# Optimization experiments

Measured on AMD Instinct MI355X. Metric: run time of the kernel, lower is better.

Reference implementation:

```python
import jax, jax.numpy as jnp
import numpy as np

N_DFT = 512
N_FILTER = N_DFT // 2 + 1  # 257
N_HOP = N_DFT // 2         # 256
AMIN = 1e-10
DYNAMIC_RANGE = 80.0


def _dft_kernels(n_dft):
    """Windowed real-DFT kernels, shape (n_dft, n_filter) each."""
    n_filter = n_dft // 2 + 1
    n = np.arange(n_dft)
    # periodic Hann (scipy.signal.hann(n_dft, sym=False))
    win = 0.5 - 0.5 * np.cos(2.0 * np.pi * n / n_dft)
    ang = 2.0 * np.pi * np.outer(n, np.arange(n_filter)) / n_dft  # (n_dft, n_filter)
    k_real = (np.cos(ang) * win[:, None]).astype(np.float32)
    k_imag = (np.sin(ang) * win[:, None]).astype(np.float32)
    return jnp.asarray(k_real), jnp.asarray(k_imag)


def setup_inputs() -> dict:
    key = jax.random.key(0)
    x = jax.random.normal(key, (32, 2, 262144), dtype=jnp.float32)  # (batch, ch, samples)
    k_real, k_imag = _dft_kernels(N_DFT)
    return {"x": x, "k_real": k_real, "k_imag": k_imag}


def reference(x, k_real, k_imag):
    n_dft = k_real.shape[0]
    n_hop = n_dft // 2
    B, C, L = x.shape
    # TF/Keras 'same' padding with stride n_hop
    n_frame = -(-L // n_hop)
    rem = L % n_hop
    pad_total = max(n_dft - n_hop, 0) if rem == 0 else max(n_dft - rem, 0)
    pad_l = pad_total // 2
    xp = jnp.pad(x, ((0, 0), (0, 0), (pad_l, pad_total - pad_l)))
    # frame the signal: (B, C, n_frame, n_dft)
    idx = jnp.arange(n_frame)[:, None] * n_hop + jnp.arange(n_dft)[None, :]
    frames = xp[:, :, idx]
    # DFT via dense GEMM with cos/sin kernels
    re = jnp.einsum('bctd,df->bctf', frames, k_real)
    im = jnp.einsum('bctd,df->bctf', frames, k_imag)
    power = re * re + im * im  # (B, C, n_frame, n_filter)
    # channels_last output: (B, n_freq, n_time, n_ch)
    out = jnp.transpose(power, (0, 3, 2, 1))
    # power_spectrogram == 2.0 -> no pow adjustment; decibel conversion:
    log10 = jnp.float32(np.log(10.0))
    log_spec = 10.0 * jnp.log(jnp.maximum(out, AMIN)) / log10
    log_spec = log_spec - jnp.max(log_spec)
    return jnp.maximum(log_spec, -DYNAMIC_RANGE)
```

## Files before the change

### kernel.cpp

```cpp
#include <hip/hip_runtime.h>
#include <math.h>

#define L_IN     262144
#define N_FRAME  1024
#define AMIN     1e-10f
#define DRANGE   80.0f
#define UNITS_CH 1056
#define WS_HI_OFF   4096
#define WS_HALF     524288
#define N4_OUT   ((32 * 257 * 1024 * 2) / 4)

typedef short bf16x8 __attribute__((ext_vector_type(8)));
typedef short bf16x4 __attribute__((ext_vector_type(4)));
typedef float f32x16 __attribute__((ext_vector_type(16)));

__device__ __forceinline__ short f2bf(float f) {
    unsigned u = __float_as_uint(f);
    u = (u + 0x7FFFu + ((u >> 16) & 1u)) >> 16;
    return (short)u;
}
__device__ __forceinline__ float bf2f(short h) {
    return __uint_as_float(((unsigned)(unsigned short)h) << 16);
}
__device__ __forceinline__ int swz(int u) { return u ^ ((u >> 5) & 7); }

__global__ __launch_bounds__(256) void wconv_kernel(
    const float* __restrict__ kr, const float* __restrict__ ki,
    short* __restrict__ whi, short* __restrict__ wlo, unsigned* __restrict__ wsmax)
{
    if (blockIdx.x == 0 && threadIdx.x == 0) wsmax[0] = 0u;
    const int tid  = threadIdx.x;
    const int pair = blockIdx.x * 4 + (tid >> 6);
    const int lane = tid & 63;
    const int fi = pair >> 5, kk = pair & 31;
    const int g = fi >> 1, nf = fi & 1;
    const int n  = lane & 31;
    const int k0 = kk * 16 + (lane >> 5) * 8;
    const int f  = g * 32 + n;
    bf16x8 h8, l8;
    #pragma unroll
    for (int j = 0; j < 8; ++j) {
        const int k = k0 + j;
        float w;
        if (nf == 1 && g == 0 && n == 0) w = kr[k * 257 + 256];
        else                             w = (nf ? ki : kr)[k * 257 + f];
        short hh = f2bf(w);
        h8[j] = hh;
        l8[j] = f2bf(w - bf2f(hh));
    }
    const int off = ((fi * 32 + kk) * 64 + lane) * 8;
    *(bf16x8*)(whi + off) = h8;
    *(bf16x8*)(wlo + off) = l8;
}

__global__ __launch_bounds__(512, 4) void spec_kernel(
    const float* __restrict__ x,
    const short* __restrict__ whi, const short* __restrict__ wlo,
    float* __restrict__ out, unsigned* __restrict__ wsmax)
{
    __shared__ __align__(16) char smem[2 * 2 * UNITS_CH * 8 * sizeof(short)];
    __shared__ float wmax[8];
    short* Ah = (short*)smem;
    short* Al = (short*)(smem + 2 * UNITS_CH * 8 * sizeof(short));
    float* S  = (float*)smem;

    const int blk = blockIdx.x;
    const int tt  = blk & 31;
    const int b   = blk >> 5;
    const int tid = threadIdx.x;
    const int lane = tid & 63;
    const int g    = tid >> 6;
    const int col  = lane & 31;
    const int half = lane >> 5;

    const int s_origin = tt * 8192 - 128;
    for (int cc = g; cc < 66; cc += 8) {
        const int ch   = (cc >= 33) ? 1 : 0;
        const int c    = cc - ch * 33;
        const int base = s_origin + c * 256;
        const float* xp = x + ((size_t)b * 2 + ch) * L_IN;
        const int i4 = base + lane * 4;
        float v[4];
        if (base >= 0 && base + 256 <= L_IN) {
            float4 p = *(const float4*)(xp + i4);
            v[0] = p.x; v[1] = p.y; v[2] = p.z; v[3] = p.w;
        } else {
            #pragma unroll
            for (int j = 0; j < 4; ++j) {
                const int idx = i4 + j;
                v[j] = (idx >= 0 && idx < L_IN) ? xp[idx] : 0.0f;
            }
        }
        bf16x4 h4, l4;
        #pragma unroll
        for (int j = 0; j < 4; ++j) {
            short hh = f2bf(v[j]);
            h4[j] = hh;
            l4[j] = f2bf(v[j] - bf2f(hh));
        }
        const int u = c * 32 + (lane >> 1);
        const int e = (ch * UNITS_CH + swz(u)) * 8 + (lane & 1) * 4;
        *(bf16x4*)&Ah[e] = h4;
        *(bf16x4*)&Al[e] = l4;
    }
    __syncthreads();

    f32x16 acc[2][2];
    #pragma unroll
    for (int mf = 0; mf < 2; ++mf)
        #pragma unroll
        for (int nf = 0; nf < 2; ++nf)
            #pragma unroll
            for (int r = 0; r < 16; ++r) acc[mf][nf][r] = 0.0f;

    const int laneoff = lane * 8;
    const short* whiW = whi + (g * 2) * 32 * 64 * 8 + laneoff;
    const short* wloW = wlo + (g * 2) * 32 * 64 * 8 + laneoff;

    for (int kk = 0; kk < 32; ++kk) {
        const int u0 = col * 32 + kk * 2 + half;
        const int e0 = swz(u0) * 8;
        const int e1 = (UNITS_CH + swz(u0)) * 8;
        const int wo = kk * 64 * 8;
        bf16x8 bh0 = *(const bf16x8*)(whiW + wo);
        bf16x8 bh1 = *(const bf16x8*)(whiW + 32 * 64 * 8 + wo);
        bf16x8 ah0 = *(const bf16x8*)&Ah[e0];
        bf16x8 ah1 = *(const bf16x8*)&Ah[e1];
        acc[0][0] = __builtin_amdgcn_mfma_f32_32x32x16_bf16(ah0, bh0, acc[0][0], 0, 0, 0);
        acc[0][1] = __builtin_amdgcn_mfma_f32_32x32x16_bf16(ah0, bh1, acc[0][1], 0, 0, 0);
        acc[1][0] = __builtin_amdgcn_mfma_f32_32x32x16_bf16(ah1, bh0, acc[1][0], 0, 0, 0);
        acc[1][1] = __builtin_amdgcn_mfma_f32_32x32x16_bf16(ah1, bh1, acc[1][1], 0, 0, 0);
        bf16x8 bl0 = *(const bf16x8*)(wloW + wo);
        bf16x8 bl1 = *(const bf16x8*)(wloW + 32 * 64 * 8 + wo);
        acc[0][0] = __builtin_amdgcn_mfma_f32_32x32x16_bf16(ah0, bl0, acc[0][0], 0, 0, 0);
        acc[0][1] = __builtin_amdgcn_mfma_f32_32x32x16_bf16(ah0, bl1, acc[0][1], 0, 0, 0);
        acc[1][0] = __builtin_amdgcn_mfma_f32_32x32x16_bf16(ah1, bl0, acc[1][0], 0, 0, 0);
        acc[1][1] = __builtin_amdgcn_mfma_f32_32x32x16_bf16(ah1, bl1, acc[1][1], 0, 0, 0);
        bf16x8 al0 = *(const bf16x8*)&Al[e0];
        bf16x8 al1 = *(const bf16x8*)&Al[e1];
        acc[0][0] = __builtin_amdgcn_mfma_f32_32x32x16_bf16(al0, bh0, acc[0][0], 0, 0, 0);
        acc[0][1] = __builtin_amdgcn_mfma_f32_32x32x16_bf16(al0, bh1, acc[0][1], 0, 0, 0);
        acc[1][0] = __builtin_amdgcn_mfma_f32_32x32x16_bf16(al1, bh0, acc[1][0], 0, 0, 0);
        acc[1][1] = __builtin_amdgcn_mfma_f32_32x32x16_bf16(al1, bh1, acc[1][1], 0, 0, 0);
    }

    __syncthreads();
    const bool nyq = (g == 0) && (col == 0);
    float pmax = 0.0f;
    #pragma unroll
    for (int mf = 0; mf < 2; ++mf) {
        #pragma unroll
        for (int r = 0; r < 16; ++r) {
            const int m   = (r & 3) + 8 * (r >> 2) + 4 * half;
            const int row = m * 2 + mf;
            const float re = acc[mf][0][r];
            const float im = acc[mf][1][r];
            const float imq = nyq ? 0.0f : im;
            float p = fmaxf(re * re + imq * imq, AMIN);
            pmax = fmaxf(pmax, p);
            S[row * 257 + g * 32 + col] = p;
            if (nyq) {
                float pn = fmaxf(im * im, AMIN);
                pmax = fmaxf(pmax, pn);
                S[row * 257 + 256] = pn;
            }
        }
    }
    #pragma unroll
    for (int off = 32; off > 0; off >>= 1)
        pmax = fmaxf(pmax, __shfl_down(pmax, off, 64));
    if (lane == 0) wmax[g] = pmax;
    __syncthreads();
    if (tid == 0) {
        float m2 = wmax[0];
        #pragma unroll
        for (int w = 1; w < 8; ++w) m2 = fmaxf(m2, wmax[w]);
        atomicMax(wsmax, __float_as_uint(m2));
    }
    float* obase = out + (size_t)b * 526336 + (size_t)tt * 64;
    for (int q = tid; q < 257 * 16; q += 512) {
        const int f = q >> 4, part = q & 15;
        float4 vv;
        vv.x = S[(part * 4 + 0) * 257 + f];
        vv.y = S[(part * 4 + 1) * 257 + f];
        vv.z = S[(part * 4 + 2) * 257 + f];
        vv.w = S[(part * 4 + 3) * 257 + f];
        *(float4*)(obase + (size_t)f * 2048 + part * 4) = vv;
    }
}

__global__ __launch_bounds__(256) void finalize_kernel(
    float* __restrict__ out, const unsigned* __restrict__ ws_max, int n4)
{
    const int i = blockIdx.x * 256 + threadIdx.x;
    if (i >= n4) return;
    const float mlog = 10.0f * log10f(__uint_as_float(*ws_max));
    float4 p = ((const float4*)out)[i];
    float4 v;
    v.x = fmaxf(10.0f * log10f(p.x) - mlog, -DRANGE);
    v.y = fmaxf(10.0f * log10f(p.y) - mlog, -DRANGE);
    v.z = fmaxf(10.0f * log10f(p.z) - mlog, -DRANGE);
    v.w = fmaxf(10.0f * log10f(p.w) - mlog, -DRANGE);
    ((float4*)out)[i] = v;
}

extern "C" void kernel_launch(void* const* d_in, const int* in_sizes, int n_in,
                              void* d_out, int out_size, void* d_ws, size_t ws_size,
                              hipStream_t stream) {
    const float* x  = (const float*)d_in[0];
    const float* kr = (const float*)d_in[1];
    const float* ki = (const float*)d_in[2];
    float* out      = (float*)d_out;

    unsigned* wsmax = (unsigned*)d_ws;
    short* whi      = (short*)((char*)d_ws + WS_HI_OFF);
    short* wlo      = (short*)((char*)d_ws + WS_HI_OFF + WS_HALF);

    wconv_kernel<<<128, 256, 0, stream>>>(kr, ki, whi, wlo, wsmax);

    const int nblocks = 32 * 32;
    spec_kernel<<<nblocks, 512, 0, stream>>>(x, whi, wlo, out, wsmax);

    const int n4 = N4_OUT;
    finalize_kernel<<<(n4 + 255) / 256, 256, 0, stream>>>(out, wsmax, n4);
}
```

Before: 214.6 us.

## Stream DFT weight tiles into LDS via async global_load_lds pipeline

Weight fragments are no longer read straight from global memory inside the MFMA loop. Each wave now issues direct global-to-LDS loads (global_load_lds) ahead of use, with a 3-stage ring for the hi weights and a 2-stage ring for the lo weights, and waits with a manual vmcnt. This is meant to hide global load latency behind the MFMA work. LDS use grows to about 146 KB and the occupancy hint in launch_bounds is dropped, so fewer blocks fit per CU. The loop also prefetches wrapped indices on the last iterations, which wastes some loads.

```diff
diff --git a/kernel.cpp b/kernel.cpp
--- a/kernel.cpp
+++ b/kernel.cpp
@@ -10,9 +10,20 @@
 #define WS_HALF     524288
 #define N4_OUT   ((32 * 257 * 1024 * 2) / 4)
 
+#define A_BYTES   67584
+#define WH_OFF    67584
+#define WL_OFF    116736
+#define SMEM_BYTES 149504
+
 typedef short bf16x8 __attribute__((ext_vector_type(8)));
 typedef short bf16x4 __attribute__((ext_vector_type(4)));
 typedef float f32x16 __attribute__((ext_vector_type(16)));
+
+typedef __attribute__((address_space(1))) const void av1_t;
+typedef __attribute__((address_space(3))) void av3_t;
+__device__ __forceinline__ void gload_lds16(const void* g, void* l) {
+    __builtin_amdgcn_global_load_lds((av1_t*)g, (av3_t*)l, 16, 0, 0);
+}
 
 __device__ __forceinline__ short f2bf(float f) {
     unsigned u = __float_as_uint(f);
@@ -53,15 +64,15 @@
     *(bf16x8*)(wlo + off) = l8;
 }
 
-__global__ __launch_bounds__(512, 4) void spec_kernel(
+__global__ __launch_bounds__(512) void spec_kernel(
     const float* __restrict__ x,
     const short* __restrict__ whi, const short* __restrict__ wlo,
     float* __restrict__ out, unsigned* __restrict__ wsmax)
 {
-    __shared__ __align__(16) char smem[2 * 2 * UNITS_CH * 8 * sizeof(short)];
+    __shared__ __align__(16) char smem[SMEM_BYTES];
     __shared__ float wmax[8];
     short* Ah = (short*)smem;
-    short* Al = (short*)(smem + 2 * UNITS_CH * 8 * sizeof(short));
+    short* Al = (short*)(smem + A_BYTES / 2);
     float* S  = (float*)smem;
 
     const int blk = blockIdx.x;
@@ -72,6 +83,16 @@
     const int g    = tid >> 6;
     const int col  = lane & 31;
     const int half = lane >> 5;
+
+    const short* wgH = whi + (g * 2) * 32 * 64 * 8 + lane * 8;
+    const short* wgL = wlo + (g * 2) * 32 * 64 * 8 + lane * 8;
+
+    gload_lds16(wgL,                 smem + WL_OFF + ((g * 2 + 0) * 2 + 0) * 1024);
+    gload_lds16(wgL + 16384,         smem + WL_OFF + ((g * 2 + 0) * 2 + 1) * 1024);
+    gload_lds16(wgH,                 smem + WH_OFF + ((g * 3 + 0) * 2 + 0) * 1024);
+    gload_lds16(wgH + 16384,         smem + WH_OFF + ((g * 3 + 0) * 2 + 1) * 1024);
+    gload_lds16(wgH + 512,           smem + WH_OFF + ((g * 3 + 1) * 2 + 0) * 1024);
+    gload_lds16(wgH + 16384 + 512,   smem + WH_OFF + ((g * 3 + 1) * 2 + 1) * 1024);
 
     const int s_origin = tt * 8192 - 128;
     for (int cc = g; cc < 66; cc += 8) {
@@ -113,35 +134,47 @@
             #pragma unroll
             for (int r = 0; r < 16; ++r) acc[mf][nf][r] = 0.0f;
 
-    const int laneoff = lane * 8;
-    const short* whiW = whi + (g * 2) * 32 * 64 * 8 + laneoff;
-    const short* wloW = wlo + (g * 2) * 32 * 64 * 8 + laneoff;
-
-    for (int kk = 0; kk < 32; ++kk) {
-        const int u0 = col * 32 + kk * 2 + half;
+    int d3 = 0;
+    for (int s = 0; s < 32; ++s) {
+        const int kkL = (s + 1) & 31;
+        const int kkH = (s + 2) & 31;
+        const int dL = (s + 1) & 1;
+        const int dH = (d3 == 0) ? 2 : d3 - 1;
+        gload_lds16(wgL + kkL * 512,         smem + WL_OFF + ((g * 2 + dL) * 2 + 0) * 1024);
+        gload_lds16(wgL + 16384 + kkL * 512, smem + WL_OFF + ((g * 2 + dL) * 2 + 1) * 1024);
+        gload_lds16(wgH + kkH * 512,         smem + WH_OFF + ((g * 3 + dH) * 2 + 0) * 1024);
+        gload_lds16(wgH + 16384 + kkH * 512, smem + WH_OFF + ((g * 3 + dH) * 2 + 1) * 1024);
+        asm volatile("s_waitcnt vmcnt(6)" ::: "memory");
+
+        const int hbase = WH_OFF + (g * 3 + d3) * 2048 + lane * 16;
+        const int lbase = WL_OFF + (g * 2 + (s & 1)) * 2048 + lane * 16;
+        bf16x8 bh0 = *(const bf16x8*)(smem + hbase);
+        bf16x8 bh1 = *(const bf16x8*)(smem + hbase + 1024);
+        bf16x8 bl0 = *(const bf16x8*)(smem + lbase);
+        bf16x8 bl1 = *(const bf16x8*)(smem + lbase + 1024);
+
+        const int u0 = col * 32 + s * 2 + half;
         const int e0 = swz(u0) * 8;
         const int e1 = (UNITS_CH + swz(u0)) * 8;
-        const int wo = kk * 64 * 8;
-        bf16x8 bh0 = *(const bf16x8*)(whiW + wo);
-        bf16x8 bh1 = *(const bf16x8*)(whiW + 32 * 64 * 8 + wo);
         bf16x8 ah0 = *(const bf16x8*)&Ah[e0];
         bf16x8 ah1 = *(const bf16x8*)&Ah[e1];
+        bf16x8 al0 = *(const bf16x8*)&Al[e0];
+        bf16x8 al1 = *(const bf16x8*)&Al[e1];
+
         acc[0][0] = __builtin_amdgcn_mfma_f32_32x32x16_bf16(ah0, bh0, acc[0][0], 0, 0, 0);
         acc[0][1] = __builtin_amdgcn_mfma_f32_32x32x16_bf16(ah0, bh1, acc[0][1], 0, 0, 0);
         acc[1][0] = __builtin_amdgcn_mfma_f32_32x32x16_bf16(ah1, bh0, acc[1][0], 0, 0, 0);
         acc[1][1] = __builtin_amdgcn_mfma_f32_32x32x16_bf16(ah1, bh1, acc[1][1], 0, 0, 0);
-        bf16x8 bl0 = *(const bf16x8*)(wloW + wo);
-        bf16x8 bl1 = *(const bf16x8*)(wloW + 32 * 64 * 8 + wo);
         acc[0][0] = __builtin_amdgcn_mfma_f32_32x32x16_bf16(ah0, bl0, acc[0][0], 0, 0, 0);
         acc[0][1] = __builtin_amdgcn_mfma_f32_32x32x16_bf16(ah0, bl1, acc[0][1], 0, 0, 0);
         acc[1][0] = __builtin_amdgcn_mfma_f32_32x32x16_bf16(ah1, bl0, acc[1][0], 0, 0, 0);
         acc[1][1] = __builtin_amdgcn_mfma_f32_32x32x16_bf16(ah1, bl1, acc[1][1], 0, 0, 0);
-        bf16x8 al0 = *(const bf16x8*)&Al[e0];
-        bf16x8 al1 = *(const bf16x8*)&Al[e1];
         acc[0][0] = __builtin_amdgcn_mfma_f32_32x32x16_bf16(al0, bh0, acc[0][0], 0, 0, 0);
         acc[0][1] = __builtin_amdgcn_mfma_f32_32x32x16_bf16(al0, bh1, acc[0][1], 0, 0, 0);
         acc[1][0] = __builtin_amdgcn_mfma_f32_32x32x16_bf16(al1, bh0, acc[1][0], 0, 0, 0);
         acc[1][1] = __builtin_amdgcn_mfma_f32_32x32x16_bf16(al1, bh1, acc[1][1], 0, 0, 0);
+
+        d3 = (d3 == 2) ? 0 : d3 + 1;
     }
 
     __syncthreads();
```

Result: slower. 242.3 us (+12.9%).

## Double-buffer weight and signal K-slices in LDS via async global-to-LDS loads

Applied to the files above, without the earlier changes.

The main loop now streams K-slices instead of staging the whole signal tile up front and reading weights straight from global memory in the MFMA loop. Weights are staged into an LDS double-buffer with global_load_lds, and each next signal slice is loaded and split into bf16 hi/lo during the current step's MFMAs. This targets global-load latency on the weight operands and the serial prologue. The cost is a barrier every K step, a smaller-footprint but different LDS layout without swizzling (possible bank conflicts), and dropping the occupancy hint in launch_bounds.

```diff
diff --git a/kernel.cpp b/kernel.cpp
--- a/kernel.cpp
+++ b/kernel.cpp
@@ -5,14 +5,22 @@
 #define N_FRAME  1024
 #define AMIN     1e-10f
 #define DRANGE   80.0f
-#define UNITS_CH 1056
 #define WS_HI_OFF   4096
 #define WS_HALF     524288
 #define N4_OUT   ((32 * 257 * 1024 * 2) / 4)
 
+#define ARING_OFF 0
+#define WRING_OFF 8192
+#define SMEM_BYTES 73728
+
 typedef short bf16x8 __attribute__((ext_vector_type(8)));
-typedef short bf16x4 __attribute__((ext_vector_type(4)));
 typedef float f32x16 __attribute__((ext_vector_type(16)));
+
+typedef __attribute__((address_space(1))) const void av1_t;
+typedef __attribute__((address_space(3))) void av3_t;
+__device__ __forceinline__ void gload_lds16(const void* g, void* l) {
+    __builtin_amdgcn_global_load_lds((av1_t*)g, (av3_t*)l, 16, 0, 0);
+}
 
 __device__ __forceinline__ short f2bf(float f) {
     unsigned u = __float_as_uint(f);
@@ -22,7 +30,6 @@
 __device__ __forceinline__ float bf2f(short h) {
     return __uint_as_float(((unsigned)(unsigned short)h) << 16);
 }
-__device__ __forceinline__ int swz(int u) { return u ^ ((u >> 5) & 7); }
 
 __global__ __launch_bounds__(256) void wconv_kernel(
     const float* __restrict__ kr, const float* __restrict__ ki,
@@ -53,16 +60,14 @@
     *(bf16x8*)(wlo + off) = l8;
 }
 
-__global__ __launch_bounds__(512, 4) void spec_kernel(
+__global__ __launch_bounds__(512) void spec_kernel(
     const float* __restrict__ x,
     const short* __restrict__ whi, const short* __restrict__ wlo,
     float* __restrict__ out, unsigned* __restrict__ wsmax)
 {
-    __shared__ __align__(16) char smem[2 * 2 * UNITS_CH * 8 * sizeof(short)];
+    __shared__ __align__(16) char smem[SMEM_BYTES];
     __shared__ float wmax[8];
-    short* Ah = (short*)smem;
-    short* Al = (short*)(smem + 2 * UNITS_CH * 8 * sizeof(short));
-    float* S  = (float*)smem;
+    float* S = (float*)smem;
 
     const int blk = blockIdx.x;
     const int tt  = blk & 31;
@@ -73,37 +78,43 @@
     const int col  = lane & 31;
     const int half = lane >> 5;
 
+    const short* wgH = whi + (g * 2) * 32 * 64 * 8 + lane * 8;
+    const short* wgL = wlo + (g * 2) * 32 * 64 * 8 + lane * 8;
+
     const int s_origin = tt * 8192 - 128;
-    for (int cc = g; cc < 66; cc += 8) {
-        const int ch   = (cc >= 33) ? 1 : 0;
-        const int c    = cc - ch * 33;
-        const int base = s_origin + c * 256;
-        const float* xp = x + ((size_t)b * 2 + ch) * L_IN;
-        const int i4 = base + lane * 4;
-        float v[4];
-        if (base >= 0 && base + 256 <= L_IN) {
-            float4 p = *(const float4*)(xp + i4);
-            v[0] = p.x; v[1] = p.y; v[2] = p.z; v[3] = p.w;
-        } else {
-            #pragma unroll
-            for (int j = 0; j < 4; ++j) {
-                const int idx = i4 + j;
-                v[j] = (idx >= 0 && idx < L_IN) ? xp[idx] : 0.0f;
-            }
-        }
-        bf16x4 h4, l4;
-        #pragma unroll
-        for (int j = 0; j < 4; ++j) {
-            short hh = f2bf(v[j]);
-            h4[j] = hh;
-            l4[j] = f2bf(v[j] - bf2f(hh));
-        }
-        const int u = c * 32 + (lane >> 1);
-        const int e = (ch * UNITS_CH + swz(u)) * 8 + (lane & 1) * 4;
-        *(bf16x4*)&Ah[e] = h4;
-        *(bf16x4*)&Al[e] = l4;
-    }
-    __syncthreads();
+    const int q    = tid >> 2;
+    const int j2   = (tid & 3) * 2;
+    const int mfst = q >> 6;
+    const int cc   = q & 63;
+    const int ubase = (cc >> 1) * 32 + (cc & 1);
+    const float* xst = x + ((size_t)b * 2 + mfst) * L_IN;
+    const int ibase = s_origin + ubase * 8 + j2;
+    const int a_waddr = q * 16 + (tid & 3) * 4;
+    const int ard0 = (col * 2 + half) * 16;
+    const int ard1 = (64 + col * 2 + half) * 16;
+
+    {
+        char* wb = smem + WRING_OFF + g * 4096;
+        gload_lds16(wgH,         wb);
+        gload_lds16(wgH + 16384, wb + 1024);
+        gload_lds16(wgL,         wb + 2048);
+        gload_lds16(wgL + 16384, wb + 3072);
+        const int i0 = ibase;
+        const bool o0 = (i0 >= 0) && (i0 < L_IN);
+        const bool o1 = (i0 + 1 >= 0) && (i0 + 1 < L_IN);
+        const int c0 = i0 < 0 ? 0 : (i0 >= L_IN ? L_IN - 1 : i0);
+        const int c1 = (i0 + 1) < 0 ? 0 : ((i0 + 1) >= L_IN ? L_IN - 1 : (i0 + 1));
+        float v0 = xst[c0]; if (!o0) v0 = 0.0f;
+        float v1 = xst[c1]; if (!o1) v1 = 0.0f;
+        short h0 = f2bf(v0), h1 = f2bf(v1);
+        short l0 = f2bf(v0 - bf2f(h0)), l1 = f2bf(v1 - bf2f(h1));
+        *(unsigned*)(smem + ARING_OFF + a_waddr) =
+            (unsigned)(unsigned short)h0 | ((unsigned)(unsigned short)h1 << 16);
+        *(unsigned*)(smem + ARING_OFF + 2048 + a_waddr) =
+            (unsigned)(unsigned short)l0 | ((unsigned)(unsigned short)l1 << 16);
+        asm volatile("s_waitcnt lgkmcnt(0)" ::: "memory");
+        __builtin_amdgcn_s_barrier();
+    }
 
     f32x16 acc[2][2];
     #pragma unroll
@@ -113,35 +124,62 @@
             #pragma unroll
             for (int r = 0; r < 16; ++r) acc[mf][nf][r] = 0.0f;
 
-    const int laneoff = lane * 8;
-    const short* whiW = whi + (g * 2) * 32 * 64 * 8 + laneoff;
-    const short* wloW = wlo + (g * 2) * 32 * 64 * 8 + laneoff;
-
-    for (int kk = 0; kk < 32; ++kk) {
-        const int u0 = col * 32 + kk * 2 + half;
-        const int e0 = swz(u0) * 8;
-        const int e1 = (UNITS_CH + swz(u0)) * 8;
-        const int wo = kk * 64 * 8;
-        bf16x8 bh0 = *(const bf16x8*)(whiW + wo);
-        bf16x8 bh1 = *(const bf16x8*)(whiW + 32 * 64 * 8 + wo);
-        bf16x8 ah0 = *(const bf16x8*)&Ah[e0];
-        bf16x8 ah1 = *(const bf16x8*)&Ah[e1];
+    int cur = 0;
+    for (int s = 0; s < 32; ++s) {
+        const int kkn = (s + 1) & 31;
+        const int nxt = cur ^ 1;
+        const int i0 = ibase + kkn * 16;
+        const bool o0 = (i0 >= 0) && (i0 < L_IN);
+        const bool o1 = (i0 + 1 >= 0) && (i0 + 1 < L_IN);
+        const int c0 = i0 < 0 ? 0 : (i0 >= L_IN ? L_IN - 1 : i0);
+        const int c1 = (i0 + 1) < 0 ? 0 : ((i0 + 1) >= L_IN ? L_IN - 1 : (i0 + 1));
+        const float v0 = xst[c0];
+        const float v1 = xst[c1];
+        {
+            char* wb = smem + WRING_OFF + (nxt * 8 + g) * 4096;
+            const short* wh = wgH + kkn * 512;
+            const short* wl = wgL + kkn * 512;
+            gload_lds16(wh,          wb);
+            gload_lds16(wh + 16384,  wb + 1024);
+            gload_lds16(wl,          wb + 2048);
+            gload_lds16(wl + 16384,  wb + 3072);
+        }
+        asm volatile("s_waitcnt vmcnt(6)" ::: "memory");
+        const char* wr = smem + WRING_OFF + (cur * 8 + g) * 4096 + lane * 16;
+        bf16x8 bh0 = *(const bf16x8*)(wr);
+        bf16x8 bh1 = *(const bf16x8*)(wr + 1024);
+        bf16x8 bl0 = *(const bf16x8*)(wr + 2048);
+        bf16x8 bl1 = *(const bf16x8*)(wr + 3072);
+        const char* ar = smem + ARING_OFF + cur * 4096;
+        bf16x8 ah0 = *(const bf16x8*)(ar + ard0);
+        bf16x8 ah1 = *(const bf16x8*)(ar + ard1);
+        bf16x8 al0 = *(const bf16x8*)(ar + 2048 + ard0);
+        bf16x8 al1 = *(const bf16x8*)(ar + 2048 + ard1);
         acc[0][0] = __builtin_amdgcn_mfma_f32_32x32x16_bf16(ah0, bh0, acc[0][0], 0, 0, 0);
         acc[0][1] = __builtin_amdgcn_mfma_f32_32x32x16_bf16(ah0, bh1, acc[0][1], 0, 0, 0);
         acc[1][0] = __builtin_amdgcn_mfma_f32_32x32x16_bf16(ah1, bh0, acc[1][0], 0, 0, 0);
         acc[1][1] = __builtin_amdgcn_mfma_f32_32x32x16_bf16(ah1, bh1, acc[1][1], 0, 0, 0);
-        bf16x8 bl0 = *(const bf16x8*)(wloW + wo);
-        bf16x8 bl1 = *(const bf16x8*)(wloW + 32 * 64 * 8 + wo);
         acc[0][0] = __builtin_amdgcn_mfma_f32_32x32x16_bf16(ah0, bl0, acc[0][0], 0, 0, 0);
         acc[0][1] = __builtin_amdgcn_mfma_f32_32x32x16_bf16(ah0, bl1, acc[0][1], 0, 0, 0);
         acc[1][0] = __builtin_amdgcn_mfma_f32_32x32x16_bf16(ah1, bl0, acc[1][0], 0, 0, 0);
         acc[1][1] = __builtin_amdgcn_mfma_f32_32x32x16_bf16(ah1, bl1, acc[1][1], 0, 0, 0);
-        bf16x8 al0 = *(const bf16x8*)&Al[e0];
-        bf16x8 al1 = *(const bf16x8*)&Al[e1];
         acc[0][0] = __builtin_amdgcn_mfma_f32_32x32x16_bf16(al0, bh0, acc[0][0], 0, 0, 0);
         acc[0][1] = __builtin_amdgcn_mfma_f32_32x32x16_bf16(al0, bh1, acc[0][1], 0, 0, 0);
         acc[1][0] = __builtin_amdgcn_mfma_f32_32x32x16_bf16(al1, bh0, acc[1][0], 0, 0, 0);
         acc[1][1] = __builtin_amdgcn_mfma_f32_32x32x16_bf16(al1, bh1, acc[1][1], 0, 0, 0);
+        {
+            float w0 = o0 ? v0 : 0.0f;
+            float w1 = o1 ? v1 : 0.0f;
+            short h0 = f2bf(w0), h1 = f2bf(w1);
+            short l0 = f2bf(w0 - bf2f(h0)), l1 = f2bf(w1 - bf2f(h1));
+            *(unsigned*)(smem + ARING_OFF + nxt * 4096 + a_waddr) =
+                (unsigned)(unsigned short)h0 | ((unsigned)(unsigned short)h1 << 16);
+            *(unsigned*)(smem + ARING_OFF + nxt * 4096 + 2048 + a_waddr) =
+                (unsigned)(unsigned short)l0 | ((unsigned)(unsigned short)l1 << 16);
+        }
+        asm volatile("s_waitcnt lgkmcnt(0)" ::: "memory");
+        __builtin_amdgcn_s_barrier();
+        cur = nxt;
     }
 
     __syncthreads();
@@ -178,8 +216,8 @@
         atomicMax(wsmax, __float_as_uint(m2));
     }
     float* obase = out + (size_t)b * 526336 + (size_t)tt * 64;
-    for (int q = tid; q < 257 * 16; q += 512) {
-        const int f = q >> 4, part = q & 15;
+    for (int qq = tid; qq < 257 * 16; qq += 512) {
+        const int f = qq >> 4, part = qq & 15;
         float4 vv;
         vv.x = S[(part * 4 + 0) * 257 + f];
         vv.y = S[(part * 4 + 1) * 257 + f];
```

Result: slower. 229.9 us (+7.1%).
